# Performance work log

Measured on AMD Instinct MI355X. Metric: run time of the kernel, lower is better.

The kernel has to match this reference:

```python
import jax, jax.numpy as jnp
import numpy as np

B, S, D, H = 4, 2048, 512, 8
DEPTH = D // H
EPS = 1e-6

def setup_inputs() -> dict:
    key = jax.random.key(0)
    ks = jax.random.split(key, 5)
    scale = 1.0 / np.sqrt(D)
    return {
        "x": jax.random.normal(ks[0], (B, S, D), dtype=jnp.float32),
        "wq": jax.random.normal(ks[1], (D, D), dtype=jnp.float32) * scale,
        "wk": jax.random.normal(ks[2], (D, D), dtype=jnp.float32) * scale,
        "wv": jax.random.normal(ks[3], (D, D), dtype=jnp.float32) * scale,
        "wo": jax.random.normal(ks[4], (D, D), dtype=jnp.float32) * scale,
        "bo": jnp.zeros((D,), dtype=jnp.float32),
        "gamma": jnp.ones((D,), dtype=jnp.float32),
        "beta": jnp.zeros((D,), dtype=jnp.float32),
    }

def _split_heads(t):
    # [B,S,D] -> [B,H,S,depth]
    return t.reshape(B, S, H, DEPTH).transpose(0, 2, 1, 3)

def reference(x, wq, wk, wv, wo, bo, gamma, beta):
    q = _split_heads(x @ wq)
    k = _split_heads(x @ wk)
    v = _split_heads(x @ wv)
    logits = jnp.einsum("bhqd,bhkd->bhqk", q, k) / jnp.sqrt(jnp.float32(DEPTH))
    attn = jax.nn.softmax(logits, axis=-1)  # dropout is identity at inference
    ctx = jnp.einsum("bhqk,bhkd->bhqd", attn, v)
    ctx = ctx.transpose(0, 2, 1, 3).reshape(B, S, D)
    out = ctx @ wo + bo
    resid = x + out  # output dropout identity at inference
    mu = jnp.mean(resid, axis=-1, keepdims=True)
    var = jnp.mean(jnp.square(resid - mu), axis=-1, keepdims=True)
    return (resid - mu) / jnp.sqrt(var + EPS) * gamma + beta
```

## Files before the change

### kernel.cpp

```cpp
#include <hip/hip_runtime.h>
#include <hip/hip_bf16.h>

typedef __attribute__((ext_vector_type(8))) short short8;
typedef __attribute__((ext_vector_type(4))) float f32x4;

constexpr int B_ = 4, S_ = 2048, D_ = 512, H_ = 8, DP_ = 64;
constexpr int M_ = B_ * S_;

__device__ __forceinline__ unsigned short f2b(float f) {
    __hip_bfloat16 h = __float2bfloat16(f);
    return *reinterpret_cast<unsigned short*>(&h);
}

__device__ __forceinline__ void gload_lds16(const unsigned short* g, unsigned short* l) {
    __builtin_amdgcn_global_load_lds((const __attribute__((address_space(1))) void*)g,
                                     (__attribute__((address_space(3))) void*)l, 16, 0, 0);
}

#define MFMA16(a, b, c) __builtin_amdgcn_mfma_f32_16x16x32_bf16((a), (b), (c), 0, 0, 0)
#define ASM_BAR() asm volatile("s_barrier" ::: "memory")

__global__ __launch_bounds__(256)
void prep(const float* __restrict__ x, unsigned short* __restrict__ xb,
          const float* __restrict__ w0, const float* __restrict__ w1,
          const float* __restrict__ w2, const float* __restrict__ w3,
          unsigned short* __restrict__ outw) {
    __shared__ float t[64][65];
    int bx = blockIdx.x;
    int tid = threadIdx.x;
    if (bx < 4096) {
        int i = bx * 256 + tid;
        float4 v = ((const float4*)x)[i];
        ushort4 o;
        o.x = f2b(v.x); o.y = f2b(v.y); o.z = f2b(v.z); o.w = f2b(v.w);
        ((ushort4*)xb)[i] = o;
        return;
    }
    int b = bx - 4096;
    int z = b >> 6, r = b & 63;
    int k0 = (r >> 3) * 64, n0 = (r & 7) * 64;
    const float* in = (z == 0) ? w0 : (z == 1) ? w1 : (z == 2) ? w2 : w3;
    unsigned short* out = outw + (size_t)z * D_ * D_;
    int tx = tid & 63, ty = tid >> 6;
#pragma unroll
    for (int i = 0; i < 16; i++) {
        int rr = ty * 16 + i;
        t[rr][tx] = in[(size_t)(k0 + rr) * D_ + n0 + tx];
    }
    __syncthreads();
#pragma unroll
    for (int i = 0; i < 16; i++) {
        int rr = ty * 16 + i;
        out[(size_t)(n0 + rr) * D_ + k0 + tx] = f2b(t[tx][rr]);
    }
}

__global__ __launch_bounds__(256, 3)
void gemm_qkvv(const unsigned short* __restrict__ X,
               const unsigned short* __restrict__ Wt,
               unsigned short* __restrict__ QKV,
               unsigned short* __restrict__ Vt) {
    int z = blockIdx.z;
    int tid = threadIdx.x;
    int wave = tid >> 6, lane = tid & 63, l16 = lane & 15, quad = lane >> 4;
    int wm = (wave >> 1) * 64, wn = (wave & 1) * 64;

    int m0, n0, bb = 0;
    const unsigned short *Abase, *Bbase;
    if (z < 2) {
        m0 = blockIdx.x * 128; n0 = blockIdx.y * 128;
        Abase = X + (size_t)m0 * D_;
        Bbase = Wt + (size_t)z * D_ * D_ + (size_t)n0 * D_;
    } else {
        int idx = blockIdx.y * 64 + blockIdx.x;
        bb = idx >> 6;
        int r = idx & 63;
        m0 = (r & 3) * 128;
        n0 = (r >> 2) * 128;
        Abase = Wt + 2 * (size_t)D_ * D_ + (size_t)m0 * D_;
        Bbase = X + ((size_t)bb * S_ + n0) * D_;
    }

    __shared__ __align__(16) unsigned short SM[17408];
    unsigned short (*As)[64] = reinterpret_cast<unsigned short(*)[64]>(SM);
    unsigned short (*Bs)[64] = reinterpret_cast<unsigned short(*)[64]>(SM + 8192);
    unsigned short (*Cs)[136] = reinterpret_cast<unsigned short(*)[136]>(SM);

    const int psw = l16 & 7;
    const int drow = lane >> 3;
    const int dsw = (lane & 7) ^ drow;

    f32x4 acc[4][4];
    const f32x4 zf = {0.f, 0.f, 0.f, 0.f};
#pragma unroll
    for (int i = 0; i < 4; i++)
#pragma unroll
        for (int j = 0; j < 4; j++) acc[i][j] = zf;

    for (int k0 = 0; k0 < D_; k0 += 64) {
        __syncthreads();
#pragma unroll
        for (int j = 0; j < 4; j++) {
            int r8 = wave * 32 + j * 8;
            gload_lds16(Abase + (size_t)(r8 + drow) * D_ + k0 + dsw * 8, &As[r8][0]);
            gload_lds16(Bbase + (size_t)(r8 + drow) * D_ + k0 + dsw * 8, &Bs[r8][0]);
        }
        __syncthreads();
#pragma unroll
        for (int h = 0; h < 2; h++) {
            short8 af[4], bf[4];
#pragma unroll
            for (int mt = 0; mt < 4; mt++)
                af[mt] = *(const short8*)&As[wm + mt * 16 + l16][((h * 4 + quad) ^ psw) * 8];
#pragma unroll
            for (int nt = 0; nt < 4; nt++)
                bf[nt] = *(const short8*)&Bs[wn + nt * 16 + l16][((h * 4 + quad) ^ psw) * 8];
#pragma unroll
            for (int nt = 0; nt < 4; nt++)
#pragma unroll
                for (int mt = 0; mt < 4; mt++)
                    acc[nt][mt] = MFMA16(bf[nt], af[mt], acc[nt][mt]);
        }
    }
    __syncthreads();
#pragma unroll
    for (int nt = 0; nt < 4; nt++)
#pragma unroll
        for (int mt = 0; mt < 4; mt++) {
            ushort4 pk;
            pk.x = f2b(acc[nt][mt][0]); pk.y = f2b(acc[nt][mt][1]);
            pk.z = f2b(acc[nt][mt][2]); pk.w = f2b(acc[nt][mt][3]);
            *(ushort4*)&Cs[wm + mt * 16 + l16][wn + nt * 16 + quad * 4] = pk;
        }
    __syncthreads();
    if (z < 2) {
        unsigned short* out = QKV + (size_t)z * M_ * D_;
#pragma unroll
        for (int i = 0; i < 8; i++) {
            int c = tid + i * 256;
            int ml = c >> 4, nch = c & 15;
            int m = m0 + ml, n = n0 + nch * 8;
            int b2 = m >> 11, ss = m & 2047, hh = n >> 6, dd = n & 63;
            *(short8*)(out + ((((size_t)b2 * H_ + hh) * S_ + ss) * DP_ + dd)) =
                *(const short8*)&Cs[ml][nch * 8];
        }
    } else {
#pragma unroll
        for (int i = 0; i < 8; i++) {
            int c = tid + i * 256;
            int ml = c >> 4, nch = c & 15;
            *(short8*)(Vt + ((size_t)bb * D_ + m0 + ml) * S_ + n0 + nch * 8) =
                *(const short8*)&Cs[ml][nch * 8];
        }
    }
}

__global__ __launch_bounds__(256, 4)
void flash_attn(const unsigned short* __restrict__ Qg, const unsigned short* __restrict__ Kg,
                const unsigned short* __restrict__ Vt, unsigned short* __restrict__ ctx) {
    int bid0 = blockIdx.x;
    int bid = (bid0 & 7) * 128 + (bid0 >> 3);
    int qt = bid & 31, hh = (bid >> 5) & 7, bb = bid >> 8;
    int tid = threadIdx.x;
    int wave = tid >> 6, lane = tid & 63, l16 = lane & 15, quad = lane >> 4;
    int qh = quad >> 1, ql = quad & 1;

    size_t bh = ((size_t)bb * H_ + hh) * S_ * DP_;
    const unsigned short* Qb = Qg + bh;
    const unsigned short* Kb = Kg + bh;
    const unsigned short* Vb = Vt + bh;

    __shared__ __align__(16) unsigned short Kls[2][64][64];
    __shared__ __align__(16) unsigned short Vls[2][64][64];
    __shared__ __align__(16) unsigned short Ps[4][16][64];

    const int psw = l16 & 7;
    const int drow = (lane >> 3) & 7;
    const int dsw = (lane & 7) ^ drow;

    short8 qf0, qf1;
    {
        const unsigned short* qp = Qb + (size_t)(qt * 64 + wave * 16 + l16) * DP_ + quad * 8;
        qf0 = *(const short8*)qp;
        qf1 = *(const short8*)(qp + 32);
    }

    auto stage = [&](int kv, int b) {
#pragma unroll
        for (int j = 0; j < 2; j++) {
            int r8 = (wave * 2 + j) * 8;
            int r = r8 + drow;
            gload_lds16(Kb + (size_t)(kv + r) * DP_ + dsw * 8, &Kls[b][r8][0]);
            gload_lds16(Vb + (size_t)r * S_ + kv + dsw * 8,    &Vls[b][r8][0]);
        }
    };

    stage(0, 0);
    stage(64, 1);
    asm volatile("s_waitcnt vmcnt(4)" ::: "memory");
    ASM_BAR();

    const f32x4 zf = {0.f, 0.f, 0.f, 0.f};
    f32x4 oacc[4];
#pragma unroll
    for (int i = 0; i < 4; i++) oacc[i] = zf;
    float m2 = -1e30f;
    float lrow = 0.f;
    constexpr float c1 = 0.125f * 1.44269504088896f;

    int cur = 0;
    for (int t = 0; t < 32; t++) {
        __builtin_amdgcn_s_setprio(1);
        f32x4 sacc[4];
#pragma unroll
        for (int nt = 0; nt < 4; nt++) {
            const unsigned short* kr = &Kls[cur][nt * 16 + l16][0];
            short8 kf0 = *(const short8*)(kr + ((quad ^ psw) * 8));
            short8 kf1 = *(const short8*)(kr + (((quad ^ 4) ^ psw) * 8));
            f32x4 s = zf;
            s = MFMA16(kf0, qf0, s);
            s = MFMA16(kf1, qf1, s);
            sacc[nt] = s;
        }
        __builtin_amdgcn_s_setprio(0);

        float t4[4];
#pragma unroll
        for (int nt = 0; nt < 4; nt++)
            t4[nt] = fmaxf(fmaxf(sacc[nt][0], sacc[nt][1]), fmaxf(sacc[nt][2], sacc[nt][3]));
        float g = fmaxf(fmaxf(t4[0], t4[1]), fmaxf(t4[2], t4[3]));
        g = fmaxf(g, __shfl_xor(g, 16));
        g = fmaxf(g, __shfl_xor(g, 32));
        g *= c1;
        float alpha = 1.0f;
        bool need = !__all(g <= m2 + 8.0f);
        if (need) {
            float m2n = fmaxf(m2, g);
            alpha = __builtin_amdgcn_exp2f(m2 - m2n);
            m2 = m2n;
        }
        float rs = 0.f;
#pragma unroll
        for (int nt = 0; nt < 4; nt++) {
            float p0 = __builtin_amdgcn_exp2f(__builtin_fmaf(sacc[nt][0], c1, -m2));
            float p1 = __builtin_amdgcn_exp2f(__builtin_fmaf(sacc[nt][1], c1, -m2));
            float p2 = __builtin_amdgcn_exp2f(__builtin_fmaf(sacc[nt][2], c1, -m2));
            float p3 = __builtin_amdgcn_exp2f(__builtin_fmaf(sacc[nt][3], c1, -m2));
            rs += (p0 + p1) + (p2 + p3);
            ushort4 pk;
            pk.x = f2b(p0); pk.y = f2b(p1); pk.z = f2b(p2); pk.w = f2b(p3);
            int c8 = (2 * nt + qh) ^ psw;
            *(ushort4*)&Ps[wave][l16][c8 * 8 + 4 * ql] = pk;
        }
        rs += __shfl_xor(rs, 16);
        rs += __shfl_xor(rs, 32);
        lrow = alpha * lrow + rs;
        if (need) {
            float al0 = __shfl(alpha, quad * 4 + 0);
            float al1 = __shfl(alpha, quad * 4 + 1);
            float al2 = __shfl(alpha, quad * 4 + 2);
            float al3 = __shfl(alpha, quad * 4 + 3);
#pragma unroll
            for (int ot = 0; ot < 4; ot++) {
                oacc[ot][0] *= al0; oacc[ot][1] *= al1;
                oacc[ot][2] *= al2; oacc[ot][3] *= al3;
            }
        }

        __builtin_amdgcn_s_setprio(1);
#pragma unroll
        for (int kt = 0; kt < 2; kt++) {
            int pc = ((kt * 4 + quad) ^ psw) * 8;
            short8 pf = *(const short8*)&Ps[wave][l16][pc];
#pragma unroll
            for (int ot = 0; ot < 4; ot++) {
                short8 vf = *(const short8*)&Vls[cur][ot * 16 + l16][pc];
                oacc[ot] = MFMA16(pf, vf, oacc[ot]);
            }
        }
        __builtin_amdgcn_s_setprio(0);

        ASM_BAR();
        if (t < 30) {
            stage((t + 2) * 64, cur);
            asm volatile("s_waitcnt vmcnt(4)" ::: "memory");
        } else {
            asm volatile("s_waitcnt vmcnt(0)" ::: "memory");
        }
        ASM_BAR();
        cur ^= 1;
    }

    float lb0 = __shfl(lrow, quad * 4 + 0);
    float lb1 = __shfl(lrow, quad * 4 + 1);
    float lb2 = __shfl(lrow, quad * 4 + 2);
    float lb3 = __shfl(lrow, quad * 4 + 3);
    float iv0 = __builtin_amdgcn_rcpf(lb0);
    float iv1 = __builtin_amdgcn_rcpf(lb1);
    float iv2 = __builtin_amdgcn_rcpf(lb2);
    float iv3 = __builtin_amdgcn_rcpf(lb3);
#pragma unroll
    for (int ot = 0; ot < 4; ot++) {
        int srow0 = qt * 64 + wave * 16 + quad * 4;
        size_t base = ((size_t)bb * S_ + srow0) * D_ + hh * DP_ + ot * 16 + l16;
        ctx[base]          = f2b(oacc[ot][0] * iv0);
        ctx[base + D_]     = f2b(oacc[ot][1] * iv1);
        ctx[base + 2 * D_] = f2b(oacc[ot][2] * iv2);
        ctx[base + 3 * D_] = f2b(oacc[ot][3] * iv3);
    }
}

__global__ __launch_bounds__(256, 3)
void gemm_proj(const unsigned short* __restrict__ A,
               const unsigned short* __restrict__ Bt,
               float* __restrict__ outf) {
    int m0 = blockIdx.x * 128, n0 = blockIdx.y * 128;
    int tid = threadIdx.x;
    int wave = tid >> 6, lane = tid & 63, l16 = lane & 15, quad = lane >> 4;
    int wm = (wave >> 1) * 64, wn = (wave & 1) * 64;

    __shared__ __align__(16) unsigned short As[128][64];
    __shared__ __align__(16) unsigned short Bs[128][64];

    const int psw = l16 & 7;
    const int drow = lane >> 3;
    const int dsw = (lane & 7) ^ drow;

    f32x4 acc[4][4];
    const f32x4 zf = {0.f, 0.f, 0.f, 0.f};
#pragma unroll
    for (int i = 0; i < 4; i++)
#pragma unroll
        for (int j = 0; j < 4; j++) acc[i][j] = zf;

    for (int k0 = 0; k0 < D_; k0 += 64) {
        __syncthreads();
#pragma unroll
        for (int j = 0; j < 4; j++) {
            int r8 = wave * 32 + j * 8;
            gload_lds16(A  + (size_t)(m0 + r8 + drow) * D_ + k0 + dsw * 8, &As[r8][0]);
            gload_lds16(Bt + (size_t)(n0 + r8 + drow) * D_ + k0 + dsw * 8, &Bs[r8][0]);
        }
        __syncthreads();
#pragma unroll
        for (int h = 0; h < 2; h++) {
            short8 af[4], bf[4];
#pragma unroll
            for (int mt = 0; mt < 4; mt++)
                af[mt] = *(const short8*)&As[wm + mt * 16 + l16][((h * 4 + quad) ^ psw) * 8];
#pragma unroll
            for (int nt = 0; nt < 4; nt++)
                bf[nt] = *(const short8*)&Bs[wn + nt * 16 + l16][((h * 4 + quad) ^ psw) * 8];
#pragma unroll
            for (int nt = 0; nt < 4; nt++)
#pragma unroll
                for (int mt = 0; mt < 4; mt++)
                    acc[nt][mt] = MFMA16(bf[nt], af[mt], acc[nt][mt]);
        }
    }
#pragma unroll
    for (int nt = 0; nt < 4; nt++)
#pragma unroll
        for (int mt = 0; mt < 4; mt++) {
            int m = m0 + wm + mt * 16 + l16;
            int n = n0 + wn + nt * 16 + quad * 4;
            *(f32x4*)&outf[(size_t)m * D_ + n] = acc[nt][mt];
        }
}

__global__ __launch_bounds__(256, 8)
void ln_out(const float* __restrict__ tmp, const float* __restrict__ Xg,
            const float* __restrict__ bo, const float* __restrict__ gamma,
            const float* __restrict__ beta, float* __restrict__ outp) {
    int wave = threadIdx.x >> 6, lane = threadIdx.x & 63;
    int row = blockIdx.x * 4 + wave;
    const float4* t4 = (const float4*)(tmp + (size_t)row * D_);
    const float4* x4 = (const float4*)(Xg + (size_t)row * D_);
    const float4* b4 = (const float4*)bo;
    const float4* g4 = (const float4*)gamma;
    const float4* e4 = (const float4*)beta;
    float4* o4 = (float4*)(outp + (size_t)row * D_);

    float4 r[2];
    float sum = 0.f, sq = 0.f;
#pragma unroll
    for (int i = 0; i < 2; i++) {
        int c = lane + i * 64;
        float4 a = t4[c], x = x4[c], b = b4[c];
        r[i].x = a.x + x.x + b.x;
        r[i].y = a.y + x.y + b.y;
        r[i].z = a.z + x.z + b.z;
        r[i].w = a.w + x.w + b.w;
        sum += (r[i].x + r[i].y) + (r[i].z + r[i].w);
        sq += (r[i].x * r[i].x + r[i].y * r[i].y) + (r[i].z * r[i].z + r[i].w * r[i].w);
    }
#pragma unroll
    for (int off = 1; off < 64; off <<= 1) {
        sum += __shfl_xor(sum, off);
        sq += __shfl_xor(sq, off);
    }
    float mu = sum * (1.0f / D_);
    float var = sq * (1.0f / D_) - mu * mu;
    float rstd = rsqrtf(var + 1e-6f);
#pragma unroll
    for (int i = 0; i < 2; i++) {
        int c = lane + i * 64;
        float4 g = g4[c], e = e4[c];
        float4 o;
        o.x = (r[i].x - mu) * rstd * g.x + e.x;
        o.y = (r[i].y - mu) * rstd * g.y + e.y;
        o.z = (r[i].z - mu) * rstd * g.z + e.z;
        o.w = (r[i].w - mu) * rstd * g.w + e.w;
        o4[c] = o;
    }
}

extern "C" void kernel_launch(void* const* d_in, const int* in_sizes, int n_in,
                              void* d_out, int out_size, void* d_ws, size_t ws_size,
                              hipStream_t stream) {
    const float* x     = (const float*)d_in[0];
    const float* wq    = (const float*)d_in[1];
    const float* wk    = (const float*)d_in[2];
    const float* wv    = (const float*)d_in[3];
    const float* wo    = (const float*)d_in[4];
    const float* bo    = (const float*)d_in[5];
    const float* gamma = (const float*)d_in[6];
    const float* beta  = (const float*)d_in[7];
    float* out = (float*)d_out;

    unsigned short* xb  = (unsigned short*)d_ws;
    unsigned short* wt  = xb + (size_t)M_ * D_;
    unsigned short* Q   = wt + 4 * D_ * D_;
    unsigned short* K   = Q + (size_t)M_ * D_;
    unsigned short* Vt  = K + (size_t)M_ * D_;
    unsigned short* ctx = xb;
    float* tmp = (float*)Q;

    prep<<<dim3(4096 + 256), 256, 0, stream>>>(x, xb, wq, wk, wv, wo, wt);
    gemm_qkvv<<<dim3(64, 4, 3), 256, 0, stream>>>(xb, wt, Q, Vt);
    flash_attn<<<dim3(1024), 256, 0, stream>>>(Q, K, Vt, ctx);
    gemm_proj<<<dim3(64, 4), 256, 0, stream>>>(ctx, wt + 3 * (size_t)D_ * D_, tmp);
    ln_out<<<dim3(2048), 256, 0, stream>>>(tmp, x, bo, gamma, beta, out);
}
```

Baseline: 190.9 us.

## Process two 16-row query sub-tiles per wave in flash attention

```diff
diff --git a/kernel.cpp b/kernel.cpp
--- a/kernel.cpp
+++ b/kernel.cpp
@@ -155,12 +155,12 @@
     }
 }
 
-__global__ __launch_bounds__(256, 4)
+__global__ __launch_bounds__(256, 3)
 void flash_attn(const unsigned short* __restrict__ Qg, const unsigned short* __restrict__ Kg,
                 const unsigned short* __restrict__ Vt, unsigned short* __restrict__ ctx) {
     int bid0 = blockIdx.x;
-    int bid = (bid0 & 7) * 128 + (bid0 >> 3);
-    int qt = bid & 31, hh = (bid >> 5) & 7, bb = bid >> 8;
+    int bid = (bid0 & 7) * 64 + (bid0 >> 3);
+    int qt = bid & 15, hh = (bid >> 4) & 7, bb = bid >> 7;
     int tid = threadIdx.x;
     int wave = tid >> 6, lane = tid & 63, l16 = lane & 15, quad = lane >> 4;
     int qh = quad >> 1, ql = quad & 1;
@@ -172,17 +172,19 @@
 
     __shared__ __align__(16) unsigned short Kls[2][64][64];
     __shared__ __align__(16) unsigned short Vls[2][64][64];
-    __shared__ __align__(16) unsigned short Ps[4][16][64];
+    __shared__ __align__(16) unsigned short Ps[4][32][64];
 
     const int psw = l16 & 7;
     const int drow = (lane >> 3) & 7;
     const int dsw = (lane & 7) ^ drow;
 
-    short8 qf0, qf1;
+    short8 qa0, qa1, qb0, qb1;
     {
-        const unsigned short* qp = Qb + (size_t)(qt * 64 + wave * 16 + l16) * DP_ + quad * 8;
-        qf0 = *(const short8*)qp;
-        qf1 = *(const short8*)(qp + 32);
+        const unsigned short* qp = Qb + (size_t)(qt * 128 + wave * 32 + l16) * DP_ + quad * 8;
+        qa0 = *(const short8*)qp;
+        qa1 = *(const short8*)(qp + 32);
+        qb0 = *(const short8*)(qp + 16 * DP_);
+        qb1 = *(const short8*)(qp + 16 * DP_ + 32);
     }
 
     auto stage = [&](int kv, int b) {
@@ -201,69 +203,92 @@
     ASM_BAR();
 
     const f32x4 zf = {0.f, 0.f, 0.f, 0.f};
-    f32x4 oacc[4];
-#pragma unroll
-    for (int i = 0; i < 4; i++) oacc[i] = zf;
-    float m2 = -1e30f;
-    float lrow = 0.f;
+    f32x4 oa[4], ob[4];
+#pragma unroll
+    for (int i = 0; i < 4; i++) { oa[i] = zf; ob[i] = zf; }
+    float m2a = -1e30f, m2b = -1e30f;
+    float lsa = 0.f, lsb = 0.f;
     constexpr float c1 = 0.125f * 1.44269504088896f;
 
     int cur = 0;
     for (int t = 0; t < 32; t++) {
         __builtin_amdgcn_s_setprio(1);
-        f32x4 sacc[4];
+        f32x4 sa[4], sb[4];
 #pragma unroll
         for (int nt = 0; nt < 4; nt++) {
             const unsigned short* kr = &Kls[cur][nt * 16 + l16][0];
             short8 kf0 = *(const short8*)(kr + ((quad ^ psw) * 8));
             short8 kf1 = *(const short8*)(kr + (((quad ^ 4) ^ psw) * 8));
             f32x4 s = zf;
-            s = MFMA16(kf0, qf0, s);
-            s = MFMA16(kf1, qf1, s);
-            sacc[nt] = s;
+            s = MFMA16(kf0, qa0, s);
+            s = MFMA16(kf1, qa1, s);
+            sa[nt] = s;
+            s = zf;
+            s = MFMA16(kf0, qb0, s);
+            s = MFMA16(kf1, qb1, s);
+            sb[nt] = s;
         }
         __builtin_amdgcn_s_setprio(0);
 
-        float t4[4];
-#pragma unroll
-        for (int nt = 0; nt < 4; nt++)
-            t4[nt] = fmaxf(fmaxf(sacc[nt][0], sacc[nt][1]), fmaxf(sacc[nt][2], sacc[nt][3]));
-        float g = fmaxf(fmaxf(t4[0], t4[1]), fmaxf(t4[2], t4[3]));
-        g = fmaxf(g, __shfl_xor(g, 16));
-        g = fmaxf(g, __shfl_xor(g, 32));
-        g *= c1;
-        float alpha = 1.0f;
-        bool need = !__all(g <= m2 + 8.0f);
+        float ga, gb;
+        {
+            float ta[4], tb[4];
+#pragma unroll
+            for (int nt = 0; nt < 4; nt++) {
+                ta[nt] = fmaxf(fmaxf(sa[nt][0], sa[nt][1]), fmaxf(sa[nt][2], sa[nt][3]));
+                tb[nt] = fmaxf(fmaxf(sb[nt][0], sb[nt][1]), fmaxf(sb[nt][2], sb[nt][3]));
+            }
+            ga = fmaxf(fmaxf(ta[0], ta[1]), fmaxf(ta[2], ta[3]));
+            gb = fmaxf(fmaxf(tb[0], tb[1]), fmaxf(tb[2], tb[3]));
+        }
+        ga = fmaxf(ga, __shfl_xor(ga, 16));
+        ga = fmaxf(ga, __shfl_xor(ga, 32));
+        gb = fmaxf(gb, __shfl_xor(gb, 16));
+        gb = fmaxf(gb, __shfl_xor(gb, 32));
+        ga *= c1; gb *= c1;
+        float ala = 1.0f, alb = 1.0f;
+        bool need = !__all((ga <= m2a + 8.0f) && (gb <= m2b + 8.0f));
         if (need) {
-            float m2n = fmaxf(m2, g);
-            alpha = __builtin_amdgcn_exp2f(m2 - m2n);
-            m2 = m2n;
-        }
-        float rs = 0.f;
+            float na = fmaxf(m2a, ga), nb = fmaxf(m2b, gb);
+            ala = __builtin_amdgcn_exp2f(m2a - na);
+            alb = __builtin_amdgcn_exp2f(m2b - nb);
+            m2a = na; m2b = nb;
+        }
+        float rsa = 0.f, rsb = 0.f;
 #pragma unroll
         for (int nt = 0; nt < 4; nt++) {
-            float p0 = __builtin_amdgcn_exp2f(__builtin_fmaf(sacc[nt][0], c1, -m2));
-            float p1 = __builtin_amdgcn_exp2f(__builtin_fmaf(sacc[nt][1], c1, -m2));
-            float p2 = __builtin_amdgcn_exp2f(__builtin_fmaf(sacc[nt][2], c1, -m2));
-            float p3 = __builtin_amdgcn_exp2f(__builtin_fmaf(sacc[nt][3], c1, -m2));
-            rs += (p0 + p1) + (p2 + p3);
+            float a0 = __builtin_amdgcn_exp2f(__builtin_fmaf(sa[nt][0], c1, -m2a));
+            float a1 = __builtin_amdgcn_exp2f(__builtin_fmaf(sa[nt][1], c1, -m2a));
+            float a2 = __builtin_amdgcn_exp2f(__builtin_fmaf(sa[nt][2], c1, -m2a));
+            float a3 = __builtin_amdgcn_exp2f(__builtin_fmaf(sa[nt][3], c1, -m2a));
+            rsa += (a0 + a1) + (a2 + a3);
             ushort4 pk;
-            pk.x = f2b(p0); pk.y = f2b(p1); pk.z = f2b(p2); pk.w = f2b(p3);
+            pk.x = f2b(a0); pk.y = f2b(a1); pk.z = f2b(a2); pk.w = f2b(a3);
             int c8 = (2 * nt + qh) ^ psw;
             *(ushort4*)&Ps[wave][l16][c8 * 8 + 4 * ql] = pk;
-        }
-        rs += __shfl_xor(rs, 16);
-        rs += __shfl_xor(rs, 32);
-        lrow = alpha * lrow + rs;
+            float b0 = __builtin_amdgcn_exp2f(__builtin_fmaf(sb[nt][0], c1, -m2b));
+            float b1 = __builtin_amdgcn_exp2f(__builtin_fmaf(sb[nt][1], c1, -m2b));
+            float b2 = __builtin_amdgcn_exp2f(__builtin_fmaf(sb[nt][2], c1, -m2b));
+            float b3 = __builtin_amdgcn_exp2f(__builtin_fmaf(sb[nt][3], c1, -m2b));
+            rsb += (b0 + b1) + (b2 + b3);
+            pk.x = f2b(b0); pk.y = f2b(b1); pk.z = f2b(b2); pk.w = f2b(b3);
+            *(ushort4*)&Ps[wave][16 + l16][c8 * 8 + 4 * ql] = pk;
+        }
+        rsa += __shfl_xor(rsa, 16);
+        rsa += __shfl_xor(rsa, 32);
+        rsb += __shfl_xor(rsb, 16);
+        rsb += __shfl_xor(rsb, 32);
+        lsa = ala * lsa + rsa;
+        lsb = alb * lsb + rsb;
         if (need) {
-            float al0 = __shfl(alpha, quad * 4 + 0);
-            float al1 = __shfl(alpha, quad * 4 + 1);
-            float al2 = __shfl(alpha, quad * 4 + 2);
-            float al3 = __shfl(alpha, quad * 4 + 3);
+            float a0 = __shfl(ala, quad * 4 + 0), a1 = __shfl(ala, quad * 4 + 1);
+            float a2 = __shfl(ala, quad * 4 + 2), a3 = __shfl(ala, quad * 4 + 3);
+            float b0 = __shfl(alb, quad * 4 + 0), b1 = __shfl(alb, quad * 4 + 1);
+            float b2 = __shfl(alb, quad * 4 + 2), b3 = __shfl(alb, quad * 4 + 3);
 #pragma unroll
             for (int ot = 0; ot < 4; ot++) {
-                oacc[ot][0] *= al0; oacc[ot][1] *= al1;
-                oacc[ot][2] *= al2; oacc[ot][3] *= al3;
+                oa[ot][0] *= a0; oa[ot][1] *= a1; oa[ot][2] *= a2; oa[ot][3] *= a3;
+                ob[ot][0] *= b0; ob[ot][1] *= b1; ob[ot][2] *= b2; ob[ot][3] *= b3;
             }
         }
 
@@ -271,11 +296,13 @@
 #pragma unroll
         for (int kt = 0; kt < 2; kt++) {
             int pc = ((kt * 4 + quad) ^ psw) * 8;
-            short8 pf = *(const short8*)&Ps[wave][l16][pc];
+            short8 pfA = *(const short8*)&Ps[wave][l16][pc];
+            short8 pfB = *(const short8*)&Ps[wave][16 + l16][pc];
 #pragma unroll
             for (int ot = 0; ot < 4; ot++) {
                 short8 vf = *(const short8*)&Vls[cur][ot * 16 + l16][pc];
-                oacc[ot] = MFMA16(pf, vf, oacc[ot]);
+                oa[ot] = MFMA16(pfA, vf, oa[ot]);
+                ob[ot] = MFMA16(pfB, vf, ob[ot]);
             }
         }
         __builtin_amdgcn_s_setprio(0);
@@ -291,22 +318,27 @@
         cur ^= 1;
     }
 
-    float lb0 = __shfl(lrow, quad * 4 + 0);
-    float lb1 = __shfl(lrow, quad * 4 + 1);
-    float lb2 = __shfl(lrow, quad * 4 + 2);
-    float lb3 = __shfl(lrow, quad * 4 + 3);
-    float iv0 = __builtin_amdgcn_rcpf(lb0);
-    float iv1 = __builtin_amdgcn_rcpf(lb1);
-    float iv2 = __builtin_amdgcn_rcpf(lb2);
-    float iv3 = __builtin_amdgcn_rcpf(lb3);
+    float la0 = __shfl(lsa, quad * 4 + 0), la1 = __shfl(lsa, quad * 4 + 1);
+    float la2 = __shfl(lsa, quad * 4 + 2), la3 = __shfl(lsa, quad * 4 + 3);
+    float lb0 = __shfl(lsb, quad * 4 + 0), lb1 = __shfl(lsb, quad * 4 + 1);
+    float lb2 = __shfl(lsb, quad * 4 + 2), lb3 = __shfl(lsb, quad * 4 + 3);
+    float ia0 = __builtin_amdgcn_rcpf(la0), ia1 = __builtin_amdgcn_rcpf(la1);
+    float ia2 = __builtin_amdgcn_rcpf(la2), ia3 = __builtin_amdgcn_rcpf(la3);
+    float ib0 = __builtin_amdgcn_rcpf(lb0), ib1 = __builtin_amdgcn_rcpf(lb1);
+    float ib2 = __builtin_amdgcn_rcpf(lb2), ib3 = __builtin_amdgcn_rcpf(lb3);
+    int srow0 = qt * 128 + wave * 32 + quad * 4;
 #pragma unroll
     for (int ot = 0; ot < 4; ot++) {
-        int srow0 = qt * 64 + wave * 16 + quad * 4;
         size_t base = ((size_t)bb * S_ + srow0) * D_ + hh * DP_ + ot * 16 + l16;
-        ctx[base]          = f2b(oacc[ot][0] * iv0);
-        ctx[base + D_]     = f2b(oacc[ot][1] * iv1);
-        ctx[base + 2 * D_] = f2b(oacc[ot][2] * iv2);
-        ctx[base + 3 * D_] = f2b(oacc[ot][3] * iv3);
+        ctx[base]          = f2b(oa[ot][0] * ia0);
+        ctx[base + D_]     = f2b(oa[ot][1] * ia1);
+        ctx[base + 2 * D_] = f2b(oa[ot][2] * ia2);
+        ctx[base + 3 * D_] = f2b(oa[ot][3] * ia3);
+        size_t baseB = base + (size_t)16 * D_;
+        ctx[baseB]          = f2b(ob[ot][0] * ib0);
+        ctx[baseB + D_]     = f2b(ob[ot][1] * ib1);
+        ctx[baseB + 2 * D_] = f2b(ob[ot][2] * ib2);
+        ctx[baseB + 3 * D_] = f2b(ob[ot][3] * ib3);
     }
 }
 
@@ -438,7 +470,7 @@
 
     prep<<<dim3(4096 + 256), 256, 0, stream>>>(x, xb, wq, wk, wv, wo, wt);
     gemm_qkvv<<<dim3(64, 4, 3), 256, 0, stream>>>(xb, wt, Q, Vt);
-    flash_attn<<<dim3(1024), 256, 0, stream>>>(Q, K, Vt, ctx);
+    flash_attn<<<dim3(512), 256, 0, stream>>>(Q, K, Vt, ctx);
     gemm_proj<<<dim3(64, 4), 256, 0, stream>>>(ctx, wt + 3 * (size_t)D_ * D_, tmp);
     ln_out<<<dim3(2048), 256, 0, stream>>>(tmp, x, bo, gamma, beta, out);
 }
```

Result: no change. 187.4 us (-1.9%).
